# Kernel tuning notes

Hardware: AMD Instinct MI355X
Metric: run time of the kernel (lower is better)

The kernel has to match this reference:

```python
import jax, jax.numpy as jnp
import numpy as np

DIM = 1024
NUM_HEADS = 16
HEAD_DIM = DIM // NUM_HEADS
BATCH = 64
SEQ = 256


def rope_tables(seq_len, head_dim, dtype=jnp.float32):
    inv_freq = 1.0 / (10000.0 ** (jnp.arange(0, head_dim, 2, dtype=jnp.float32) / head_dim))
    pos = jnp.arange(seq_len, dtype=jnp.float32)
    freqs = jnp.outer(pos, inv_freq)            # (S, head_dim/2)
    emb = jnp.concatenate([freqs, freqs], -1)   # (S, head_dim)
    return jnp.cos(emb).astype(dtype), jnp.sin(emb).astype(dtype)


def rotate_half(x):
    x1, x2 = jnp.split(x, 2, axis=-1)
    return jnp.concatenate([-x2, x1], axis=-1)


def setup_inputs() -> dict:
    key = jax.random.key(0)
    ks = jax.random.split(key, 5)
    x = jax.random.normal(ks[0], (BATCH, SEQ, DIM), dtype=jnp.float32)
    mask = jnp.ones((BATCH, SEQ), dtype=jnp.int32)
    s = 1.0 / np.sqrt(DIM)
    Wq = jax.random.normal(ks[1], (DIM, DIM), dtype=jnp.float32) * s
    Wk = jax.random.normal(ks[2], (DIM, DIM), dtype=jnp.float32) * s
    Wv = jax.random.normal(ks[3], (DIM, DIM), dtype=jnp.float32) * s
    Wo = jax.random.normal(ks[4], (DIM, DIM), dtype=jnp.float32) * s
    return {"x": x, "mask": mask, "Wq": Wq, "Wk": Wk, "Wv": Wv, "Wo": Wo}


def reference(x, mask, Wq, Wk, Wv, Wo):
    B, S, D = x.shape
    H, Hd = NUM_HEADS, HEAD_DIM
    scale = Hd ** -0.5
    # torch nn.Linear: y = x @ W^T  (weights stored as (out,in))
    q = (x @ Wq.T).reshape(B, S, H, Hd).transpose(0, 2, 1, 3)  # (B,H,S,Hd)
    k = (x @ Wk.T).reshape(B, S, H, Hd).transpose(0, 2, 1, 3)
    v = (x @ Wv.T).reshape(B, S, H, Hd).transpose(0, 2, 1, 3)
    cos, sin = rope_tables(S, Hd, x.dtype)       # (S,Hd)
    cos = cos[None, None]                         # (1,1,S,Hd)
    sin = sin[None, None]
    q = q * cos + rotate_half(q) * sin
    k = k * cos + rotate_half(k) * sin
    scores = jnp.einsum('bhqd,bhkd->bhqk', q, k) * scale  # (B,H,S,S)
    m = (mask[:, None, None, :] != 0)             # (B,1,1,S)
    scores = jnp.where(m, scores, -jnp.inf)
    attn = jax.nn.softmax(scores, axis=-1)
    out = jnp.einsum('bhqk,bhkd->bhqd', attn, v)  # (B,H,S,Hd)
    out = out.transpose(0, 2, 1, 3).reshape(B, S, D)
    return out @ Wo.T
```

## Files before the change

### kernel.cpp

```cpp
#include <hip/hip_runtime.h>

typedef __attribute__((ext_vector_type(8))) short short8;
typedef __attribute__((ext_vector_type(4))) float f32x4;

#define DEV __device__ __forceinline__

DEV unsigned short f2bf(float f) {
    unsigned int u = __float_as_uint(f);
    u += 0x7FFFu + ((u >> 16) & 1u);
    return (unsigned short)(u >> 16);
}
DEV float bf2f(unsigned short h) { return __uint_as_float(((unsigned int)h) << 16); }

DEV void gload16(const void* g, void* l) {
    __builtin_amdgcn_global_load_lds(
        (const __attribute__((address_space(1))) void*)(unsigned long long)g,
        (__attribute__((address_space(3))) void*)(unsigned int)(unsigned long long)l,
        16, 0, 0);
}

__global__ void cast_bf16_kernel(const float* __restrict__ in, unsigned short* __restrict__ out, int n8) {
    int gid = blockIdx.x * 256 + threadIdx.x;
    if (gid >= n8) return;
    const f32x4* p = (const f32x4*)in + (size_t)gid * 2;
    f32x4 a = p[0], b = p[1];
    short8 v;
    v[0] = (short)f2bf(a[0]); v[1] = (short)f2bf(a[1]); v[2] = (short)f2bf(a[2]); v[3] = (short)f2bf(a[3]);
    v[4] = (short)f2bf(b[0]); v[5] = (short)f2bf(b[1]); v[6] = (short)f2bf(b[2]); v[7] = (short)f2bf(b[3]);
    *(short8*)(out + (size_t)gid * 8) = v;
}

__global__ void cast_w4_kernel(const float* __restrict__ w0, const float* __restrict__ w1,
                               const float* __restrict__ w2, const float* __restrict__ w3,
                               unsigned short* __restrict__ o0, unsigned short* __restrict__ o1,
                               unsigned short* __restrict__ o2, unsigned short* __restrict__ o3) {
    int gid = blockIdx.x * 256 + threadIdx.x;
    int sel = gid >> 17, idx = gid & 131071;
    const float* in = (sel == 0) ? w0 : (sel == 1) ? w1 : (sel == 2) ? w2 : w3;
    unsigned short* out = (sel == 0) ? o0 : (sel == 1) ? o1 : (sel == 2) ? o2 : o3;
    const f32x4* p = (const f32x4*)in + (size_t)idx * 2;
    f32x4 a = p[0], b = p[1];
    short8 v;
    v[0] = (short)f2bf(a[0]); v[1] = (short)f2bf(a[1]); v[2] = (short)f2bf(a[2]); v[3] = (short)f2bf(a[3]);
    v[4] = (short)f2bf(b[0]); v[5] = (short)f2bf(b[1]); v[6] = (short)f2bf(b[2]); v[7] = (short)f2bf(b[3]);
    *(short8*)(out + (size_t)idx * 8) = v;
}

__global__ void rope_table_kernel(float* __restrict__ cosT, float* __restrict__ sinT) {
    int gid = blockIdx.x * 256 + threadIdx.x;
    if (gid >= 256 * 32) return;
    int s = gid >> 5, i = gid & 31;
    float inv = powf(10000.0f, -(float)i * (1.0f / 32.0f));
    float f = (float)s * inv;
    cosT[gid] = cosf(f);
    sinT[gid] = sinf(f);
}

#define NT0 16

#define Ald(B, K) (SLDS + ((B) * 2 + (K)) * 8192)
#define Bld(B, K) (SLDS + 32768 + ((B) * 2 + (K)) * 8192)

#define STAGE2(SW, SBUF, SKH, TS) do {                                         \
    int ts_ = (TS) < NT0 ? (TS) : (NT0 - 1);                                   \
    const unsigned short* sp_ = SW##base + (size_t)ts_ * 64 + (SKH) * 32;      \
    gload16(sp_ + rel0, SW##ld(SBUF, SKH) + (size_t)tid * 8);                  \
    gload16(sp_ + rel1, SW##ld(SBUF, SKH) + (size_t)(tid + 512) * 8);          \
} while (0)

#define MM(MH, MI, NI)                                                         \
    acc[(MH)*4+(MI)][(NI)] = __builtin_amdgcn_mfma_f32_16x16x32_bf16(          \
        av##MI, bva[(NI)], acc[(MH)*4+(MI)][(NI)], 0, 0, 0)

#define PH0(BUF, KH, MH, SW, SBUF, SKH, TS, DW) do {                           \
    short8 av0 = *(const short8*)&Ald(BUF, KH)[aoff[(MH)*4 + 0]];              \
    short8 av1 = *(const short8*)&Ald(BUF, KH)[aoff[(MH)*4 + 1]];              \
    short8 av2 = *(const short8*)&Ald(BUF, KH)[aoff[(MH)*4 + 2]];              \
    short8 av3 = *(const short8*)&Ald(BUF, KH)[aoff[(MH)*4 + 3]];              \
    if ((MH) == 0) {                                                           \
        bva[0] = *(const short8*)&Bld(BUF, KH)[boff[0]];                       \
        bva[1] = *(const short8*)&Bld(BUF, KH)[boff[1]];                       \
        bva[2] = *(const short8*)&Bld(BUF, KH)[boff[2]];                       \
        bva[3] = *(const short8*)&Bld(BUF, KH)[boff[3]];                       \
    }                                                                          \
    STAGE2(SW, SBUF, SKH, TS);                                                 \
    if (DW) asm volatile("s_waitcnt vmcnt(8)" ::: "memory");                   \
    asm volatile("" ::: "memory");                                             \
    __builtin_amdgcn_s_barrier();                                              \
    asm volatile("" ::: "memory");                                             \
    __builtin_amdgcn_s_setprio(1);                                             \
    MM(MH,0,0); MM(MH,1,0); MM(MH,2,0); MM(MH,3,0);                            \
    MM(MH,0,1); MM(MH,1,1); MM(MH,2,1); MM(MH,3,1);                            \
    MM(MH,0,2); MM(MH,1,2); MM(MH,2,2); MM(MH,3,2);                            \
    MM(MH,0,3); MM(MH,1,3); MM(MH,2,3); MM(MH,3,3);                            \
    __builtin_amdgcn_s_setprio(0);                                             \
    asm volatile("" ::: "memory");                                             \
    __builtin_amdgcn_s_barrier();                                              \
    asm volatile("" ::: "memory");                                             \
} while (0)

#define TILE0(BUF, T)                                                          \
    PH0(BUF, 0, 0, A, (BUF)^1, 1, (T)+1, 0);                                   \
    PH0(BUF, 0, 1, B, (BUF)^1, 1, (T)+1, 1);                                   \
    PH0(BUF, 1, 0, A, (BUF),   0, (T)+2, 0);                                   \
    PH0(BUF, 1, 1, B, (BUF),   0, (T)+2, 1);

template <int MODE>
__global__ __launch_bounds__(512, 2) void gemm256_kernel(
    const unsigned short* __restrict__ A,
    const unsigned short* __restrict__ W0,
    const unsigned short* __restrict__ W1,
    const unsigned short* __restrict__ W2,
    unsigned short* __restrict__ q,
    unsigned short* __restrict__ k,
    unsigned short* __restrict__ vt,
    float* __restrict__ outF,
    const float* __restrict__ cosT,
    const float* __restrict__ sinT)
{
    __shared__ __align__(16) unsigned short SLDS[65536];

    const int tid = threadIdx.x;
    const int l = tid & 63;
    const int w = tid >> 6;
    const int wr = w >> 2, wc = w & 3;
    const int l15 = l & 15, lg = l >> 4;

    const int nwg = gridDim.x;
    const int bid = blockIdx.x;
    const int cpx = nwg >> 3;
    const int swz = (bid & 7) * cpx + (bid >> 3);
    const int NBX = (MODE == 0) ? 12 : 4;
    const int bx = swz % NBX, by = swz / NBX;
    const int m0 = by * 256, n0 = bx * 256;

    const unsigned short* Bp;
    int nb = n0, sel = 3;
    if (MODE == 0) {
        sel = n0 >> 10;
        Bp = (sel == 0) ? W0 : ((sel == 1) ? W1 : W2);
        nb = n0 & 1023;
    } else {
        Bp = W0;
    }

    const int f0 = tid, f1 = tid + 512;
    const int rel0 = (f0 >> 2) * 1024 + (((f0 & 3) ^ ((f0 >> 3) & 3)) * 8);
    const int rel1 = (f1 >> 2) * 1024 + (((f1 & 3) ^ ((f1 >> 3) & 3)) * 8);
    const unsigned short* Abase = A + (size_t)m0 * 1024;
    const unsigned short* Bbase = Bp + (size_t)nb * 1024;

    int aoff[8], boff[4];
#pragma unroll
    for (int mi = 0; mi < 8; ++mi) {
        int row = wr * 128 + mi * 16 + l15;
        aoff[mi] = row * 32 + ((lg ^ ((row >> 1) & 3)) * 8);
    }
#pragma unroll
    for (int ni = 0; ni < 4; ++ni) {
        int row = wc * 64 + ni * 16 + l15;
        boff[ni] = row * 32 + ((lg ^ ((row >> 1) & 3)) * 8);
    }

    f32x4 acc[8][4];
#pragma unroll
    for (int mi = 0; mi < 8; ++mi)
#pragma unroll
        for (int ni = 0; ni < 4; ++ni)
#pragma unroll
            for (int e = 0; e < 4; ++e) acc[mi][ni][e] = 0.f;

    short8 bva[4];

    STAGE2(A, 0, 0, 0); STAGE2(B, 0, 0, 0);
    STAGE2(A, 0, 1, 0); STAGE2(B, 0, 1, 0);
    STAGE2(A, 1, 0, 1); STAGE2(B, 1, 0, 1);
    asm volatile("s_waitcnt vmcnt(8)" ::: "memory");
    asm volatile("" ::: "memory");
    __builtin_amdgcn_s_barrier();
    asm volatile("" ::: "memory");

#pragma unroll 1
    for (int it = 0; it < NT0 / 2; ++it) {
        const int t0 = it * 2;
        TILE0(0, t0);
        TILE0(1, t0 + 1);
    }

    if (MODE == 1) {
#pragma unroll
        for (int mi = 0; mi < 8; ++mi) {
#pragma unroll
            for (int i = 0; i < 4; ++i) {
                int grow = m0 + wr * 128 + mi * 16 + lg * 4 + i;
#pragma unroll
                for (int ni = 0; ni < 4; ++ni) {
                    int col = n0 + wc * 64 + ni * 16 + l15;
                    outF[(size_t)grow * 1024 + col] = acc[mi][ni][i];
                }
            }
        }
        return;
    }

    asm volatile("s_waitcnt vmcnt(0)" ::: "memory");
    __syncthreads();

    const int b = m0 >> 8;

    if (sel < 2) {
#pragma unroll
        for (int mi = 0; mi < 8; ++mi) {
#pragma unroll
            for (int i = 0; i < 4; ++i) {
                int srow = wr * 128 + mi * 16 + lg * 4 + i;
                int s = srow & 255;
#pragma unroll
                for (int ni = 0; ni < 2; ++ni) {
                    int d = ni * 16 + l15;
                    float c = cosT[s * 32 + d], sn = sinT[s * 32 + d];
                    float lo = acc[mi][ni][i], hi = acc[mi][ni + 2][i];
                    acc[mi][ni][i] = lo * c - hi * sn;
                    acc[mi][ni + 2][i] = hi * c + lo * sn;
                }
#pragma unroll
                for (int ni = 0; ni < 4; ++ni) {
                    int col = wc * 64 + ni * 16 + l15;
                    int byte = srow * 512 + ((col * 2) ^ ((srow & 7) << 4));
                    *(unsigned short*)((char*)SLDS + byte) = f2bf(acc[mi][ni][i]);
                }
            }
        }
    } else {
#pragma unroll
        for (int mi = 0; mi < 8; ++mi) {
#pragma unroll
            for (int i = 0; i < 4; ++i) {
                int srow = wr * 128 + mi * 16 + lg * 4 + i;
#pragma unroll
                for (int ni = 0; ni < 4; ++ni) {
                    int col = wc * 64 + ni * 16 + l15;
                    int byte = col * 512 + ((srow * 2) ^ ((col & 7) << 4));
                    *(unsigned short*)((char*)SLDS + byte) = f2bf(acc[mi][ni][i]);
                }
            }
        }
    }
    __syncthreads();

    {
        const int r = tid >> 5, ct = tid & 31;
        unsigned short* dst01 = (sel == 0) ? q : k;
#pragma unroll
        for (int rg = 0; rg < 16; ++rg) {
            int row = rg * 16 + r;
            int byte = row * 512 + ((ct * 16) ^ ((row & 7) << 4));
            short8 v = *(const short8*)((char*)SLDS + byte);
            if (sel < 2) {
                int col = ct * 8;
                int h = (nb + col) >> 6, d = col & 63;
                *(short8*)(dst01 + (((size_t)(b * 16 + h) * 256 + row) * 64 + d)) = v;
            } else {
                int gc = nb + row;
                int h = gc >> 6, d = gc & 63;
                *(short8*)(vt + (((size_t)(b * 16 + h) * 64 + d) * 256 + ct * 8)) = v;
            }
        }
    }
}

__global__ __launch_bounds__(512) void attn_kernel(
    const unsigned short* __restrict__ qp,
    const unsigned short* __restrict__ kp,
    const unsigned short* __restrict__ vtp,
    const int* __restrict__ mask,
    unsigned short* __restrict__ ao)
{
    __shared__ __align__(16) unsigned short Ks[128 * 64];
    __shared__ __align__(16) unsigned short Vts[64 * 128];
    __shared__ __align__(16) unsigned short Ps[8][32 * 64];

    const int bh = blockIdx.x;
    const int b = bh >> 4, h = bh & 15;
    const int tid = threadIdx.x;
    const int l = tid & 63, w = tid >> 6;
    const int l15 = l & 15, lg = l >> 4;

    const unsigned short* kbase = kp + (size_t)bh * (256 * 64);
    const unsigned short* vtbase = vtp + (size_t)bh * (64 * 256);
    const unsigned short* qbase = qp + (size_t)bh * (256 * 64) + (size_t)(w * 32) * 64;

    short8 aq[2][2];
#pragma unroll
    for (int m = 0; m < 2; ++m)
#pragma unroll
        for (int ks = 0; ks < 2; ++ks)
            aq[m][ks] = *(const short8*)(qbase + (m * 16 + l15) * 64 + ks * 32 + lg * 8);

    float m_run[2][4], l_run[2][4];
    f32x4 o[2][4];
#pragma unroll
    for (int m = 0; m < 2; ++m)
#pragma unroll
        for (int i = 0; i < 4; ++i) { m_run[m][i] = -3.0e38f; l_run[m][i] = 0.f; }
#pragma unroll
    for (int m = 0; m < 2; ++m)
#pragma unroll
        for (int n = 0; n < 4; ++n)
#pragma unroll
            for (int e = 0; e < 4; ++e) o[m][n][e] = 0.f;

    const int* mrow = mask + b * 256;

    for (int half = 0; half < 2; ++half) {
        __syncthreads();
        for (int c2 = tid; c2 < 1024; c2 += 512) {
            int off = c2 * 16;
            int row = off >> 7, cb = off & 127;
            short8 v = *(const short8*)((const char*)kbase + (size_t)half * 16384 + off);
            *(short8*)((char*)Ks + row * 128 + (cb ^ ((row & 7) << 4))) = v;
        }
        for (int c2 = tid; c2 < 1024; c2 += 512) {
            int off = c2 * 16;
            int row = off >> 8, cb = off & 255;
            short8 v = *(const short8*)((const char*)vtbase + (size_t)row * 512 + half * 256 + cb);
            *(short8*)((char*)Vts + row * 256 + (cb ^ ((row & 7) << 4))) = v;
        }
        __syncthreads();

        for (int t2 = 0; t2 < 2; ++t2) {
            const int keyl = t2 * 64;
            const int keyg = half * 128 + keyl;

            f32x4 sf[2][4];
#pragma unroll
            for (int m = 0; m < 2; ++m)
#pragma unroll
                for (int n = 0; n < 4; ++n)
#pragma unroll
                    for (int e = 0; e < 4; ++e) sf[m][n][e] = 0.f;
#pragma unroll
            for (int ks = 0; ks < 2; ++ks) {
                short8 bk[4];
#pragma unroll
                for (int n = 0; n < 4; ++n) {
                    int row = keyl + n * 16 + l15;
                    int cb = (ks * 64 + lg * 16) ^ ((row & 7) << 4);
                    bk[n] = *(const short8*)((char*)Ks + row * 128 + cb);
                }
#pragma unroll
                for (int m = 0; m < 2; ++m)
#pragma unroll
                    for (int n = 0; n < 4; ++n)
                        sf[m][n] = __builtin_amdgcn_mfma_f32_16x16x32_bf16(aq[m][ks], bk[n], sf[m][n], 0, 0, 0);
            }
            float madd[4];
#pragma unroll
            for (int n = 0; n < 4; ++n) madd[n] = mrow[keyg + n * 16 + l15] ? 0.f : -1e30f;
#pragma unroll
            for (int m = 0; m < 2; ++m)
#pragma unroll
                for (int n = 0; n < 4; ++n)
#pragma unroll
                    for (int i = 0; i < 4; ++i) sf[m][n][i] = sf[m][n][i] * 0.125f + madd[n];
            float al[2][4];
#pragma unroll
            for (int m = 0; m < 2; ++m)
#pragma unroll
                for (int i = 0; i < 4; ++i) {
                    float mx = fmaxf(fmaxf(sf[m][0][i], sf[m][1][i]), fmaxf(sf[m][2][i], sf[m][3][i]));
                    mx = fmaxf(mx, __shfl_xor(mx, 1));
                    mx = fmaxf(mx, __shfl_xor(mx, 2));
                    mx = fmaxf(mx, __shfl_xor(mx, 4));
                    mx = fmaxf(mx, __shfl_xor(mx, 8));
                    float mnew = fmaxf(m_run[m][i], mx);
                    al[m][i] = __expf(m_run[m][i] - mnew);
                    m_run[m][i] = mnew;
                }
            float rs[2][4];
#pragma unroll
            for (int m = 0; m < 2; ++m)
#pragma unroll
                for (int i = 0; i < 4; ++i) rs[m][i] = 0.f;
#pragma unroll
            for (int m = 0; m < 2; ++m)
#pragma unroll
                for (int n = 0; n < 4; ++n)
#pragma unroll
                    for (int i = 0; i < 4; ++i) {
                        float p = __expf(sf[m][n][i] - m_run[m][i]);
                        sf[m][n][i] = p;
                        rs[m][i] += p;
                    }
#pragma unroll
            for (int m = 0; m < 2; ++m)
#pragma unroll
                for (int i = 0; i < 4; ++i) {
                    float r2 = rs[m][i];
                    r2 += __shfl_xor(r2, 1);
                    r2 += __shfl_xor(r2, 2);
                    r2 += __shfl_xor(r2, 4);
                    r2 += __shfl_xor(r2, 8);
                    l_run[m][i] = l_run[m][i] * al[m][i] + r2;
                }
#pragma unroll
            for (int m = 0; m < 2; ++m)
#pragma unroll
                for (int n = 0; n < 4; ++n)
#pragma unroll
                    for (int i = 0; i < 4; ++i) o[m][n][i] *= al[m][i];

            __syncthreads();
#pragma unroll
            for (int m = 0; m < 2; ++m)
#pragma unroll
                for (int n = 0; n < 4; ++n)
#pragma unroll
                    for (int i = 0; i < 4; ++i) {
                        int row = m * 16 + lg * 4 + i;
                        int cb = ((n * 16 + l15) * 2) ^ ((row & 7) << 4);
                        *(unsigned short*)((char*)Ps[w] + row * 128 + cb) = f2bf(sf[m][n][i]);
                    }
            __syncthreads();
#pragma unroll
            for (int ks = 0; ks < 2; ++ks) {
                short8 pa[2];
#pragma unroll
                for (int m = 0; m < 2; ++m) {
                    int row = m * 16 + l15;
                    int cb = (ks * 64 + lg * 16) ^ ((row & 7) << 4);
                    pa[m] = *(const short8*)((char*)Ps[w] + row * 128 + cb);
                }
                short8 vb[4];
#pragma unroll
                for (int n = 0; n < 4; ++n) {
                    int row = n * 16 + l15;
                    int cb = (keyl * 2 + ks * 64 + lg * 16) ^ ((row & 7) << 4);
                    vb[n] = *(const short8*)((char*)Vts + row * 256 + cb);
                }
#pragma unroll
                for (int m = 0; m < 2; ++m)
#pragma unroll
                    for (int n = 0; n < 4; ++n)
                        o[m][n] = __builtin_amdgcn_mfma_f32_16x16x32_bf16(pa[m], vb[n], o[m][n], 0, 0, 0);
            }
        }
    }

    unsigned short* aop = ao + ((size_t)(b * 256 + w * 32)) * 1024 + h * 64;
#pragma unroll
    for (int m = 0; m < 2; ++m)
#pragma unroll
        for (int n = 0; n < 4; ++n)
#pragma unroll
            for (int i = 0; i < 4; ++i) {
                int row = m * 16 + lg * 4 + i;
                int d = n * 16 + l15;
                aop[(size_t)row * 1024 + d] = f2bf(o[m][n][i] / l_run[m][i]);
            }
}

extern "C" void kernel_launch(void* const* d_in, const int* in_sizes, int n_in,
                              void* d_out, int out_size, void* d_ws, size_t ws_size,
                              hipStream_t stream) {
    const float* x = (const float*)d_in[0];
    const int* mask = (const int*)d_in[1];
    const float* Wq = (const float*)d_in[2];
    const float* Wk = (const float*)d_in[3];
    const float* Wv = (const float*)d_in[4];
    const float* Wo = (const float*)d_in[5];
    float* out = (float*)d_out;

    char* ws = (char*)d_ws;
    size_t off = 0;
    auto alloc = [&](size_t bytes) -> char* {
        char* p = ws + off;
        off = (off + bytes + 255) & ~(size_t)255;
        return p;
    };
    unsigned short* xb = (unsigned short*)alloc((size_t)16384 * 1024 * 2);
    unsigned short* wqb = (unsigned short*)alloc((size_t)1024 * 1024 * 2);
    unsigned short* wkb = (unsigned short*)alloc((size_t)1024 * 1024 * 2);
    unsigned short* wvb = (unsigned short*)alloc((size_t)1024 * 1024 * 2);
    unsigned short* wob = (unsigned short*)alloc((size_t)1024 * 1024 * 2);
    unsigned short* q = (unsigned short*)alloc((size_t)16384 * 1024 * 2);
    unsigned short* k = (unsigned short*)alloc((size_t)16384 * 1024 * 2);
    unsigned short* vt = (unsigned short*)alloc((size_t)16384 * 1024 * 2);
    float* cosT = (float*)alloc(256 * 32 * 4);
    float* sinT = (float*)alloc(256 * 32 * 4);

    cast_bf16_kernel<<<16777216 / 8 / 256, 256, 0, stream>>>(x, xb, 16777216 / 8);
    cast_w4_kernel<<<4 * 131072 / 256, 256, 0, stream>>>(Wq, Wk, Wv, Wo, wqb, wkb, wvb, wob);
    rope_table_kernel<<<32, 256, 0, stream>>>(cosT, sinT);

    gemm256_kernel<0><<<768, 512, 0, stream>>>(xb, wqb, wkb, wvb, q, k, vt, nullptr, cosT, sinT);
    attn_kernel<<<1024, 512, 0, stream>>>(q, k, vt, mask, xb );
    gemm256_kernel<1><<<256, 512, 0, stream>>>(xb, wob, nullptr, nullptr, nullptr, nullptr, nullptr, out, cosT, sinT);

    (void)in_sizes; (void)n_in; (void)out_size; (void)ws_size;
}
```

Baseline: 249.5 us.

## Merge prep kernels, stage output GEMM stores through LDS, drop attn barriers

```diff
diff --git a/kernel.cpp b/kernel.cpp
--- a/kernel.cpp
+++ b/kernel.cpp
@@ -19,41 +19,42 @@
         16, 0, 0);
 }
 
-__global__ void cast_bf16_kernel(const float* __restrict__ in, unsigned short* __restrict__ out, int n8) {
-    int gid = blockIdx.x * 256 + threadIdx.x;
-    if (gid >= n8) return;
-    const f32x4* p = (const f32x4*)in + (size_t)gid * 2;
+DEV void cast8(const float* in, unsigned short* out, size_t idx8) {
+    const f32x4* p = (const f32x4*)in + idx8 * 2;
     f32x4 a = p[0], b = p[1];
     short8 v;
     v[0] = (short)f2bf(a[0]); v[1] = (short)f2bf(a[1]); v[2] = (short)f2bf(a[2]); v[3] = (short)f2bf(a[3]);
     v[4] = (short)f2bf(b[0]); v[5] = (short)f2bf(b[1]); v[6] = (short)f2bf(b[2]); v[7] = (short)f2bf(b[3]);
-    *(short8*)(out + (size_t)gid * 8) = v;
-}
-
-__global__ void cast_w4_kernel(const float* __restrict__ w0, const float* __restrict__ w1,
-                               const float* __restrict__ w2, const float* __restrict__ w3,
-                               unsigned short* __restrict__ o0, unsigned short* __restrict__ o1,
-                               unsigned short* __restrict__ o2, unsigned short* __restrict__ o3) {
-    int gid = blockIdx.x * 256 + threadIdx.x;
-    int sel = gid >> 17, idx = gid & 131071;
-    const float* in = (sel == 0) ? w0 : (sel == 1) ? w1 : (sel == 2) ? w2 : w3;
-    unsigned short* out = (sel == 0) ? o0 : (sel == 1) ? o1 : (sel == 2) ? o2 : o3;
-    const f32x4* p = (const f32x4*)in + (size_t)idx * 2;
-    f32x4 a = p[0], b = p[1];
-    short8 v;
-    v[0] = (short)f2bf(a[0]); v[1] = (short)f2bf(a[1]); v[2] = (short)f2bf(a[2]); v[3] = (short)f2bf(a[3]);
-    v[4] = (short)f2bf(b[0]); v[5] = (short)f2bf(b[1]); v[6] = (short)f2bf(b[2]); v[7] = (short)f2bf(b[3]);
-    *(short8*)(out + (size_t)idx * 8) = v;
-}
-
-__global__ void rope_table_kernel(float* __restrict__ cosT, float* __restrict__ sinT) {
-    int gid = blockIdx.x * 256 + threadIdx.x;
-    if (gid >= 256 * 32) return;
-    int s = gid >> 5, i = gid & 31;
-    float inv = powf(10000.0f, -(float)i * (1.0f / 32.0f));
-    float f = (float)s * inv;
-    cosT[gid] = cosf(f);
-    sinT[gid] = sinf(f);
+    *(short8*)(out + idx8 * 8) = v;
+}
+
+__global__ void init_kernel(const float* __restrict__ x,
+                            const float* __restrict__ w0, const float* __restrict__ w1,
+                            const float* __restrict__ w2, const float* __restrict__ w3,
+                            unsigned short* __restrict__ xb,
+                            unsigned short* __restrict__ o0, unsigned short* __restrict__ o1,
+                            unsigned short* __restrict__ o2, unsigned short* __restrict__ o3,
+                            float* __restrict__ cosT, float* __restrict__ sinT) {
+    int blk = blockIdx.x;
+    int tid = threadIdx.x;
+    if (blk < 8192) {
+        cast8(x, xb, (size_t)blk * 256 + tid);
+    } else if (blk < 8192 + 2048) {
+        int gid = (blk - 8192) * 256 + tid;
+        int sel = gid >> 17, idx = gid & 131071;
+        const float* in = (sel == 0) ? w0 : (sel == 1) ? w1 : (sel == 2) ? w2 : w3;
+        unsigned short* out = (sel == 0) ? o0 : (sel == 1) ? o1 : (sel == 2) ? o2 : o3;
+        cast8(in, out, (size_t)idx);
+    } else {
+        int gid = (blk - 8192 - 2048) * 256 + tid;
+        if (gid < 256 * 32) {
+            int s = gid >> 5, i = gid & 31;
+            float inv = powf(10000.0f, -(float)i * (1.0f / 32.0f));
+            float f = (float)s * inv;
+            cosT[gid] = cosf(f);
+            sinT[gid] = sinf(f);
+        }
+    }
 }
 
 #define NT0 16
@@ -187,24 +188,44 @@
         TILE0(1, t0 + 1);
     }
 
-    if (MODE == 1) {
-#pragma unroll
-        for (int mi = 0; mi < 8; ++mi) {
-#pragma unroll
-            for (int i = 0; i < 4; ++i) {
-                int grow = m0 + wr * 128 + mi * 16 + lg * 4 + i;
-#pragma unroll
-                for (int ni = 0; ni < 4; ++ni) {
-                    int col = n0 + wc * 64 + ni * 16 + l15;
-                    outF[(size_t)grow * 1024 + col] = acc[mi][ni][i];
-                }
-            }
-        }
-        return;
-    }
-
     asm volatile("s_waitcnt vmcnt(0)" ::: "memory");
     __syncthreads();
+
+    if (MODE == 1) {
+        char* lds = (char*)SLDS;
+        const int lane32 = tid & 31, r16 = tid >> 5;
+#pragma unroll 1
+        for (int h2 = 0; h2 < 2; ++h2) {
+            if (wr == h2) {
+#pragma unroll
+                for (int mi = 0; mi < 8; ++mi) {
+#pragma unroll
+                    for (int i = 0; i < 4; ++i) {
+                        int rl = mi * 16 + lg * 4 + i;
+#pragma unroll
+                        for (int ni = 0; ni < 4; ++ni) {
+                            int col = wc * 64 + ni * 16 + l15;
+                            int byte = rl * 1024 + ((col * 4) ^ ((rl & 7) << 4));
+                            *(float*)(lds + byte) = acc[mi][ni][i];
+                        }
+                    }
+                }
+            }
+            __syncthreads();
+#pragma unroll
+            for (int it2 = 0; it2 < 16; ++it2) {
+                int rl = (it2 & 7) * 16 + r16;
+                int hf = it2 >> 3;
+                int byte = rl * 1024 + ((hf * 512 + lane32 * 16) ^ ((rl & 7) << 4));
+                f32x4 v = *(const f32x4*)(lds + byte);
+                int grow = m0 + h2 * 128 + rl;
+                int col = n0 + hf * 128 + lane32 * 4;
+                *(f32x4*)(outF + (size_t)grow * 1024 + col) = v;
+            }
+            __syncthreads();
+        }
+        return;
+    }
 
     const int b = m0 >> 8;
 
@@ -410,7 +431,6 @@
 #pragma unroll
                     for (int i = 0; i < 4; ++i) o[m][n][i] *= al[m][i];
 
-            __syncthreads();
 #pragma unroll
             for (int m = 0; m < 2; ++m)
 #pragma unroll
@@ -421,7 +441,6 @@
                         int cb = ((n * 16 + l15) * 2) ^ ((row & 7) << 4);
                         *(unsigned short*)((char*)Ps[w] + row * 128 + cb) = f2bf(sf[m][n][i]);
                     }
-            __syncthreads();
 #pragma unroll
             for (int ks = 0; ks < 2; ++ks) {
                 short8 pa[2];
@@ -489,9 +508,8 @@
     float* cosT = (float*)alloc(256 * 32 * 4);
     float* sinT = (float*)alloc(256 * 32 * 4);
 
-    cast_bf16_kernel<<<16777216 / 8 / 256, 256, 0, stream>>>(x, xb, 16777216 / 8);
-    cast_w4_kernel<<<4 * 131072 / 256, 256, 0, stream>>>(Wq, Wk, Wv, Wo, wqb, wkb, wvb, wob);
-    rope_table_kernel<<<32, 256, 0, stream>>>(cosT, sinT);
+    init_kernel<<<8192 + 2048 + 32, 256, 0, stream>>>(x, Wq, Wk, Wv, Wo,
+                                                      xb, wqb, wkb, wvb, wob, cosT, sinT);
 
     gemm256_kernel<0><<<768, 512, 0, stream>>>(xb, wqb, wkb, wvb, q, k, vt, nullptr, cosT, sinT);
     attn_kernel<<<1024, 512, 0, stream>>>(q, k, vt, mask, xb );
```

Measured after the change: 258.4 us. +3.6%, slower.
